# Optimization experiments

Hardware: AMD Instinct MI355X
Metric: run time of the kernel (lower is better)

## Reference

```python
import jax, jax.numpy as jnp
import numpy as np

B, N, K, H, G, C, P = 2, 8192, 16, 128, 256, 10, 8


def _w(key, fan_in, fan_out):
    return jax.random.normal(key, (fan_in, fan_out), jnp.float32) * (1.0 / np.sqrt(fan_in))


def setup_inputs() -> dict:
    key = jax.random.key(0)
    ks = jax.random.split(key, 24)
    inp = {
        "points": jax.random.normal(ks[0], (B, N, 3), jnp.float32),
        "normals": jax.random.normal(ks[1], (B, N, 3), jnp.float32),
        # point_encoder: Linear(6,H) -> ReLU -> Linear(H,H) -> ReLU
        "We1": _w(ks[2], 6, H), "be1": jnp.zeros((H,), jnp.float32),
        "We2": _w(ks[3], H, H), "be2": jnp.zeros((H,), jnp.float32),
        # local_mlp: Linear(2H,H) -> ReLU -> Linear(H,H) -> ReLU
        "Wl1": _w(ks[4], 2 * H, H), "bl1": jnp.zeros((H,), jnp.float32),
        "Wl2": _w(ks[5], H, H), "bl2": jnp.zeros((H,), jnp.float32),
        # context_proj: Linear(2H,G) -> ReLU
        "Wc": _w(ks[6], 2 * H, G), "bc": jnp.zeros((G,), jnp.float32),
        # classifier: Linear(2H+G,H) -> ReLU -> Linear(H,C)
        "Wk1": _w(ks[7], 2 * H + G, H), "bk1": jnp.zeros((H,), jnp.float32),
        "Wk2": _w(ks[8], H, C), "bk2": jnp.zeros((C,), jnp.float32),
        # param_head: Linear(2H+G,H) -> ReLU -> Linear(H,P)
        "Wp1": _w(ks[9], 2 * H + G, H), "bp1": jnp.zeros((H,), jnp.float32),
        "Wp2": _w(ks[10], H, P), "bp2": jnp.zeros((P,), jnp.float32),
        "k": K,
    }
    return inp


def _knn_indices(points, k):
    # squared pairwise distances (same ordering as torch.cdist); no grad needed
    pts = jax.lax.stop_gradient(points)
    sq = jnp.sum(pts * pts, axis=-1)                      # [B,N]
    d2 = sq[:, :, None] + sq[:, None, :] - 2.0 * jnp.einsum('bnc,bmc->bnm', pts, pts)
    _, idx = jax.lax.top_k(-d2, k + 1)                    # smallest k+1 distances
    return idx[:, :, 1:]                                  # drop self -> [B,N,k]


def _forward(points, normals, We1, be1, We2, be2, Wl1, bl1, Wl2, bl2,
             Wc, bc, Wk1, bk1, Wk2, bk2, Wp1, bp1, Wp2, bp2, k):
    x = jnp.concatenate([points, normals], axis=-1)       # [B,N,6]
    pf = jax.nn.relu(jax.nn.relu(x @ We1 + be1) @ We2 + be2)   # [B,N,H]

    idx = _knn_indices(points, k)                         # [B,N,k]
    nbr = jax.vmap(lambda f, i: f[i])(pf, idx)            # [B,N,k,H]
    ctr = pf[:, :, None, :]
    edge = jnp.concatenate([jnp.broadcast_to(ctr, nbr.shape), nbr - ctr], axis=-1)  # [B,N,k,2H]
    lf = jax.nn.relu(jax.nn.relu(edge @ Wl1 + bl1) @ Wl2 + bl2)
    lf = jnp.max(lf, axis=2)                              # [B,N,H]

    ctx = jax.nn.relu(jnp.concatenate([pf, lf], axis=-1) @ Wc + bc)  # [B,N,G]
    gf = jnp.max(ctx, axis=1, keepdims=True)              # [B,1,G]
    gf = jnp.broadcast_to(gf, (pf.shape[0], pf.shape[1], gf.shape[-1]))

    fused = jnp.concatenate([pf, lf, gf], axis=-1)        # [B,N,2H+G]
    logits = jax.nn.relu(fused @ Wk1 + bk1) @ Wk2 + bk2
    param_pred = jax.nn.relu(fused @ Wp1 + bp1) @ Wp2 + bp2
    return logits, param_pred


def reference(points, normals, We1, be1, We2, be2, Wl1, bl1, Wl2, bl2,
              Wc, bc, Wk1, bk1, Wk2, bk2, Wp1, bp1, Wp2, bp2, k):
    return _forward(points, normals, We1, be1, We2, be2, Wl1, bl1, Wl2, bl2,
                    Wc, bc, Wk1, bk1, Wk2, bk2, Wp1, bp1, Wp2, bp2, k)
```

## Files before the change

### kernel.cpp

```cpp
#include <hip/hip_runtime.h>

#define B_ 2
#define N_ 8192
#define NP 16384
#define K_ 16
#define H_ 128
#define KCAP 512

typedef short bf16x8 __attribute__((ext_vector_type(8)));
typedef float f32x4 __attribute__((ext_vector_type(4)));

__device__ inline unsigned short f2b(float f) {
    unsigned u = __builtin_bit_cast(unsigned, f);
    unsigned r = (u + 0x7fff + ((u >> 16) & 1)) >> 16;
    return (unsigned short)r;
}
__device__ inline bf16x8 ldb8(const unsigned short* p) {
    return *(const bf16x8*)p;
}
__device__ inline uint4 pack8(float4 a, float4 b) {
    uint4 pk;
    pk.x = (unsigned)f2b(a.x) | ((unsigned)f2b(a.y) << 16);
    pk.y = (unsigned)f2b(a.z) | ((unsigned)f2b(a.w) << 16);
    pk.z = (unsigned)f2b(b.x) | ((unsigned)f2b(b.y) << 16);
    pk.w = (unsigned)f2b(b.z) | ((unsigned)f2b(b.w) << 16);
    return pk;
}

__global__ __launch_bounds__(256) void k_h1(
    const float* __restrict__ pts, const float* __restrict__ nrm,
    const float* __restrict__ We1, const float* __restrict__ be1,
    unsigned short* __restrict__ h1, float* __restrict__ gf,
    float4* __restrict__ pts4) {
    int tid = blockIdx.x * 256 + threadIdx.x;
    if (blockIdx.x == 0) { gf[threadIdx.x] = 0.f; gf[256 + threadIdx.x] = 0.f; }
    if (tid < NP) {
        int p = tid;
        float x = pts[p * 3], y = pts[p * 3 + 1], z = pts[p * 3 + 2];
        float sq = __fadd_rn(__fadd_rn(__fmul_rn(x, x), __fmul_rn(y, y)), __fmul_rn(z, z));
        pts4[p] = make_float4(x, y, z, sq);
    }
    for (int o = tid; o < NP * 128; o += gridDim.x * 256) {
        int p = o >> 7, h = o & 127;
        float a = be1[h];
        a += pts[p * 3]     * We1[0 * 128 + h];
        a += pts[p * 3 + 1] * We1[1 * 128 + h];
        a += pts[p * 3 + 2] * We1[2 * 128 + h];
        a += nrm[p * 3]     * We1[3 * 128 + h];
        a += nrm[p * 3 + 1] * We1[4 * 128 + h];
        a += nrm[p * 3 + 2] * We1[5 * 128 + h];
        h1[o] = f2b(fmaxf(a, 0.f));
    }
}

__global__ __launch_bounds__(256) void k_prep(
    const float* __restrict__ Wl1, const float* __restrict__ bl1,
    const float* __restrict__ Wl2, const float* __restrict__ Wc,
    const float* __restrict__ Wk1, const float* __restrict__ Wp1,
    const float* __restrict__ We2,
    unsigned short* __restrict__ WuvT, float* __restrict__ bias_cat,
    unsigned short* __restrict__ Wl2T, unsigned short* __restrict__ WcT,
    unsigned short* __restrict__ Wk1T, unsigned short* __restrict__ Wp1T,
    unsigned short* __restrict__ We2T) {
    int tid = blockIdx.x * 256 + threadIdx.x;
    int stride = gridDim.x * 256;
    for (int i = tid; i < 256 * 128; i += stride) {
        int n = i >> 7, k = i & 127;
        float val = (n < 128) ? Wl1[k * 128 + n] - Wl1[(k + 128) * 128 + n]
                              : Wl1[(k + 128) * 128 + (n - 128)];
        WuvT[i] = f2b(val);
    }
    for (int i = tid; i < 256; i += stride) bias_cat[i] = (i < 128) ? bl1[i] : 0.f;
    for (int i = tid; i < 128 * 128; i += stride) {
        int n = i >> 7, k = i & 127;
        Wl2T[i] = f2b(Wl2[k * 128 + n]);
        We2T[i] = f2b(We2[k * 128 + n]);
    }
    for (int i = tid; i < 256 * 256; i += stride) {
        int n = i >> 8, k = i & 255;
        WcT[i] = f2b(Wc[k * 256 + n]);
    }
    for (int i = tid; i < 128 * 512; i += stride) {
        int n = i >> 9, k = i & 511;
        Wk1T[i] = f2b(Wk1[k * 128 + n]);
        Wp1T[i] = f2b(Wp1[k * 128 + n]);
    }
}

__global__ __launch_bounds__(256) void k_pf2(
    const unsigned short* __restrict__ h1, const unsigned short* __restrict__ We2T,
    const float* __restrict__ be2, float* __restrict__ pf) {
    int t = threadIdx.x, l = t & 63, w = t >> 6;
    int row0 = blockIdx.x * 64 + w * 16;
    f32x4 acc[8];
    #pragma unroll
    for (int nj = 0; nj < 8; ++nj) acc[nj] = (f32x4){0.f, 0.f, 0.f, 0.f};
    #pragma unroll
    for (int ks = 0; ks < 4; ++ks) {
        bf16x8 a = ldb8(&h1[(size_t)(row0 + (l & 15)) * 128 + ks * 32 + (l >> 4) * 8]);
        #pragma unroll
        for (int nj = 0; nj < 8; ++nj) {
            bf16x8 bfr = ldb8(&We2T[(size_t)(nj * 16 + (l & 15)) * 128 + ks * 32 + (l >> 4) * 8]);
            acc[nj] = __builtin_amdgcn_mfma_f32_16x16x32_bf16(a, bfr, acc[nj], 0, 0, 0);
        }
    }
    #pragma unroll
    for (int nj = 0; nj < 8; ++nj) {
        int col = nj * 16 + (l & 15);
        float bias = be2[col];
        #pragma unroll
        for (int rg = 0; rg < 4; ++rg) {
            int row = row0 + (l >> 4) * 4 + rg;
            pf[(size_t)row * 128 + col] = fmaxf(acc[nj][rg] + bias, 0.f);
        }
    }
}

__device__ inline float knn_thresh(const int* __restrict__ hh, int l) {
    int h0 = hh[4 * l], h1 = hh[4 * l + 1], h2 = hh[4 * l + 2], h3 = hh[4 * l + 3];
    int c0 = h0, c1 = c0 + h1, c2 = c1 + h2, c3 = c2 + h3;
    int tot = c3;
    int inc = tot;
    for (int off = 1; off < 64; off <<= 1) {
        int vv = __shfl_up(inc, off);
        if (l >= off) inc += vv;
    }
    int excl = inc - tot;
    int Bc = 255;
    if      (excl + c0 >= 16) Bc = 4 * l;
    else if (excl + c1 >= 16) Bc = 4 * l + 1;
    else if (excl + c2 >= 16) Bc = 4 * l + 2;
    else if (excl + c3 >= 16) Bc = 4 * l + 3;
    for (int m = 1; m < 64; m <<= 1) Bc = min(Bc, __shfl_xor(Bc, m));
    return __uint_as_float((unsigned)(Bc + 401) << 21);
}

__global__ __launch_bounds__(256) void k_knn(
    const float4* __restrict__ pts4, int* __restrict__ knn) {
    __shared__ int hist[4][2][260];
    __shared__ unsigned buf[4][2][KCAP];
    int t = threadIdx.x, w = t >> 6, l = t & 63;
    int b = blockIdx.x >> 10;
    int qbase = (blockIdx.x & 1023) * 8 + w * 2;
    const float4* pb = pts4 + b * N_;
    float4 qp0 = pb[qbase];
    float4 qp1 = pb[qbase + 1];
    for (int i = l; i < 520; i += 64) (&hist[w][0][0])[i] = 0;
    int cnt0 = 0, cnt1 = 0;

    float d2c0[16], d2c1[16];
    #pragma unroll
    for (int i = 0; i < 16; ++i) {
        int j = l + 64 * i;
        float4 c = pb[j];
        float dot0 = __fadd_rn(__fadd_rn(__fmul_rn(qp0.x, c.x), __fmul_rn(qp0.y, c.y)), __fmul_rn(qp0.z, c.z));
        float d20 = __fsub_rn(__fadd_rn(qp0.w, c.w), __fmul_rn(2.f, dot0));
        float dot1 = __fadd_rn(__fadd_rn(__fmul_rn(qp1.x, c.x), __fmul_rn(qp1.y, c.y)), __fmul_rn(qp1.z, c.z));
        float d21 = __fsub_rn(__fadd_rn(qp1.w, c.w), __fmul_rn(2.f, dot1));
        d2c0[i] = d20; d2c1[i] = d21;
        float hv0 = (j == qbase) ? 1e30f : d20;
        float hv1 = (j == qbase + 1) ? 1e30f : d21;
        unsigned u0 = __float_as_uint(hv0);
        int bk0 = (hv0 < 0.f) ? 0 : min(255, max(0, (int)(u0 >> 21) - 400));
        atomicAdd(&hist[w][0][bk0], 1);
        unsigned u1 = __float_as_uint(hv1);
        int bk1 = (hv1 < 0.f) ? 0 : min(255, max(0, (int)(u1 >> 21) - 400));
        atomicAdd(&hist[w][1][bk1], 1);
    }
    float Tf0 = knn_thresh(&hist[w][0][0], l);
    float Tf1 = knn_thresh(&hist[w][1][0], l);

    #pragma unroll
    for (int i = 0; i < 16; ++i) {
        int j = l + 64 * i;
        bool t0 = d2c0[i] < Tf0;
        unsigned long long m0 = __ballot(t0);
        if (t0) {
            int pos = cnt0 + __popcll(m0 & ((1ull << l) - 1ull));
            if (pos < KCAP) buf[w][0][pos] = (unsigned)j;
        }
        cnt0 += __popcll(m0);
        bool t1 = d2c1[i] < Tf1;
        unsigned long long m1 = __ballot(t1);
        if (t1) {
            int pos = cnt1 + __popcll(m1 & ((1ull << l) - 1ull));
            if (pos < KCAP) buf[w][1][pos] = (unsigned)j;
        }
        cnt1 += __popcll(m1);
    }

    #pragma unroll 2
    for (int i = 16; i < 128; ++i) {
        int j = l + 64 * i;
        float4 c = pb[j];
        float dot0 = __fadd_rn(__fadd_rn(__fmul_rn(qp0.x, c.x), __fmul_rn(qp0.y, c.y)), __fmul_rn(qp0.z, c.z));
        float d20 = __fsub_rn(__fadd_rn(qp0.w, c.w), __fmul_rn(2.f, dot0));
        float dot1 = __fadd_rn(__fadd_rn(__fmul_rn(qp1.x, c.x), __fmul_rn(qp1.y, c.y)), __fmul_rn(qp1.z, c.z));
        float d21 = __fsub_rn(__fadd_rn(qp1.w, c.w), __fmul_rn(2.f, dot1));
        bool t0 = d20 < Tf0;
        unsigned long long m0 = __ballot(t0);
        if (t0) {
            int pos = cnt0 + __popcll(m0 & ((1ull << l) - 1ull));
            if (pos < KCAP) buf[w][0][pos] = (unsigned)j;
        }
        cnt0 += __popcll(m0);
        bool t1 = d21 < Tf1;
        unsigned long long m1 = __ballot(t1);
        if (t1) {
            int pos = cnt1 + __popcll(m1 & ((1ull << l) - 1ull));
            if (pos < KCAP) buf[w][1][pos] = (unsigned)j;
        }
        cnt1 += __popcll(m1);
    }

    for (int qq = 0; qq < 2; ++qq) {
        int q = qbase + qq;
        float4 qp = qq ? qp1 : qp0;
        int m_ = min(qq ? cnt1 : cnt0, KCAP);
        unsigned long long key[8];
        #pragma unroll
        for (int r = 0; r < 8; ++r) {
            int e = l + 64 * r;
            if (e < m_) {
                int idx = (int)buf[w][qq][e];
                float4 c = pb[idx];
                float dot = __fadd_rn(__fadd_rn(__fmul_rn(qp.x, c.x), __fmul_rn(qp.y, c.y)), __fmul_rn(qp.z, c.z));
                float d2 = __fsub_rn(__fadd_rn(qp.w, c.w), __fmul_rn(2.f, dot));
                unsigned du = __float_as_uint(d2);
                unsigned mu = du ^ (unsigned)(((int)du >> 31) | 0x80000000);
                key[r] = ((unsigned long long)mu << 32) | (unsigned)idx;
            } else key[r] = ~0ull;
        }
        unsigned long long lmin = key[0];
        #pragma unroll
        for (int r = 1; r < 8; ++r) lmin = (key[r] < lmin) ? key[r] : lmin;
        int emitted = 0;
        for (int r17 = 0; r17 < 17 && emitted < 16; ++r17) {
            unsigned long long wv = lmin;
            for (int m = 1; m < 64; m <<= 1) {
                unsigned long long o = __shfl_xor(wv, m);
                wv = (o < wv) ? o : wv;
            }
            int idx = (int)(wv & 0xffffffffu);
            if (idx != q) {
                if (l == 0) knn[((size_t)b * N_ + q) * 16 + emitted] = b * N_ + idx;
                ++emitted;
            }
            if (lmin == wv) {
                #pragma unroll
                for (int r = 0; r < 8; ++r) if (key[r] == wv) key[r] = ~0ull;
                lmin = key[0];
                #pragma unroll
                for (int r = 1; r < 8; ++r) lmin = (key[r] < lmin) ? key[r] : lmin;
            }
        }
    }
}

__global__ __launch_bounds__(256) void k_uv(
    const float* __restrict__ pf, const unsigned short* __restrict__ WuvT,
    const float* __restrict__ bias_cat,
    float* __restrict__ u, float* __restrict__ v) {
    __shared__ __align__(16) unsigned short As[128 * 136];
    int t = threadIdx.x;
    int l = t & 63, w = t >> 6;
    int wr = w >> 1, wcn = w & 1;
    int rowbase = blockIdx.x * 128;
    int ncol0 = blockIdx.y * 128;

    #pragma unroll
    for (int i = 0; i < 8; ++i) {
        int ci = t + 256 * i;
        int r = ci >> 4, c8 = (ci & 15) * 8;
        const float4* sp = (const float4*)(pf + (size_t)(rowbase + r) * 128 + c8);
        *(uint4*)&As[r * 136 + c8] = pack8(sp[0], sp[1]);
    }
    __syncthreads();

    f32x4 acc[4][4];
    #pragma unroll
    for (int i = 0; i < 4; ++i)
        #pragma unroll
        for (int j = 0; j < 4; ++j) acc[i][j] = (f32x4){0.f, 0.f, 0.f, 0.f};

    #pragma unroll
    for (int ks = 0; ks < 4; ++ks) {
        bf16x8 bfr[4], afr[4];
        #pragma unroll
        for (int nj = 0; nj < 4; ++nj)
            bfr[nj] = ldb8(&WuvT[(size_t)(ncol0 + wcn * 64 + nj * 16 + (l & 15)) * 128 + ks * 32 + (l >> 4) * 8]);
        #pragma unroll
        for (int mi = 0; mi < 4; ++mi)
            afr[mi] = ldb8(&As[(wr * 64 + mi * 16 + (l & 15)) * 136 + ks * 32 + (l >> 4) * 8]);
        #pragma unroll
        for (int mi = 0; mi < 4; ++mi)
            #pragma unroll
            for (int nj = 0; nj < 4; ++nj)
                acc[mi][nj] = __builtin_amdgcn_mfma_f32_16x16x32_bf16(afr[mi], bfr[nj], acc[mi][nj], 0, 0, 0);
    }
    float* outp = (ncol0 == 0) ? u : v;
    #pragma unroll
    for (int mi = 0; mi < 4; ++mi)
        #pragma unroll
        for (int nj = 0; nj < 4; ++nj) {
            int col = wcn * 64 + nj * 16 + (l & 15);
            float bias = bias_cat[ncol0 + col];
            #pragma unroll
            for (int rg = 0; rg < 4; ++rg) {
                int row = wr * 64 + mi * 16 + (l >> 4) * 4 + rg;
                outp[(size_t)(rowbase + row) * 128 + col] = acc[mi][nj][rg] + bias;
            }
        }
}

__global__ __launch_bounds__(256) void k_edge(
    const float* __restrict__ u, const float* __restrict__ v,
    const int* __restrict__ knn, const unsigned short* __restrict__ Wl2T,
    const float* __restrict__ bl2, float* __restrict__ lf) {
    __shared__ __align__(16) unsigned short h1s[128 * 136];
    int t = threadIdx.x;
    int l = t & 63, w = t >> 6;
    int wr = w >> 1, wcn = w & 1;
    int rowbase = blockIdx.x * 128;
    int p0 = blockIdx.x * 8;

    #pragma unroll 2
    for (int i = 0; i < 8; ++i) {
        int ci = t + 256 * i;
        int r = ci >> 4, c8 = (ci & 15) * 8;
        int nb = knn[rowbase + r];
        int pt = p0 + (r >> 4);
        const float4* vp = (const float4*)(v + (size_t)nb * 128 + c8);
        const float4* up = (const float4*)(u + (size_t)pt * 128 + c8);
        float4 va = vp[0], vb = vp[1];
        float4 ua = up[0], ub = up[1];
        unsigned d0 = (unsigned)f2b(fmaxf(ua.x + va.x, 0.f)) | ((unsigned)f2b(fmaxf(ua.y + va.y, 0.f)) << 16);
        unsigned d1 = (unsigned)f2b(fmaxf(ua.z + va.z, 0.f)) | ((unsigned)f2b(fmaxf(ua.w + va.w, 0.f)) << 16);
        unsigned d2 = (unsigned)f2b(fmaxf(ub.x + vb.x, 0.f)) | ((unsigned)f2b(fmaxf(ub.y + vb.y, 0.f)) << 16);
        unsigned d3 = (unsigned)f2b(fmaxf(ub.z + vb.z, 0.f)) | ((unsigned)f2b(fmaxf(ub.w + vb.w, 0.f)) << 16);
        uint4 pk; pk.x = d0; pk.y = d1; pk.z = d2; pk.w = d3;
        *(uint4*)&h1s[r * 136 + c8] = pk;
    }
    __syncthreads();

    f32x4 acc[4][4];
    #pragma unroll
    for (int i = 0; i < 4; ++i)
        #pragma unroll
        for (int j = 0; j < 4; ++j) acc[i][j] = (f32x4){0.f, 0.f, 0.f, 0.f};

    #pragma unroll
    for (int ks = 0; ks < 4; ++ks) {
        bf16x8 bfr[4], afr[4];
        #pragma unroll
        for (int nj = 0; nj < 4; ++nj)
            bfr[nj] = ldb8(&Wl2T[(size_t)(wcn * 64 + nj * 16 + (l & 15)) * 128 + ks * 32 + (l >> 4) * 8]);
        #pragma unroll
        for (int mi = 0; mi < 4; ++mi)
            afr[mi] = ldb8(&h1s[(wr * 64 + mi * 16 + (l & 15)) * 136 + ks * 32 + (l >> 4) * 8]);
        #pragma unroll
        for (int mi = 0; mi < 4; ++mi)
            #pragma unroll
            for (int nj = 0; nj < 4; ++nj)
                acc[mi][nj] = __builtin_amdgcn_mfma_f32_16x16x32_bf16(afr[mi], bfr[nj], acc[mi][nj], 0, 0, 0);
    }

    #pragma unroll
    for (int mi = 0; mi < 4; ++mi)
        #pragma unroll
        for (int nj = 0; nj < 4; ++nj) {
            int col = wcn * 64 + nj * 16 + (l & 15);
            float bias = bl2[col];
            float m = fmaxf(acc[mi][nj][0] + bias, 0.f);
            m = fmaxf(m, fmaxf(acc[mi][nj][1] + bias, 0.f));
            m = fmaxf(m, fmaxf(acc[mi][nj][2] + bias, 0.f));
            m = fmaxf(m, fmaxf(acc[mi][nj][3] + bias, 0.f));
            m = fmaxf(m, __shfl_xor(m, 16));
            m = fmaxf(m, __shfl_xor(m, 32));
            if (l < 16) lf[(size_t)(p0 + wr * 4 + mi) * 128 + col] = m;
        }
}

__global__ __launch_bounds__(256) void k_ctx(
    const float* __restrict__ pf, const float* __restrict__ lf,
    const unsigned short* __restrict__ WcT, const float* __restrict__ bc,
    float* __restrict__ gf) {
    __shared__ __align__(16) unsigned short As[128 * 136];
    int t = threadIdx.x;
    int l = t & 63, w = t >> 6;
    int wr = w >> 1, wcn = w & 1;
    int rowbase = blockIdx.x * 128;
    int ncol0 = blockIdx.y * 128;
    int b = rowbase >> 13;

    f32x4 acc[4][4];
    #pragma unroll
    for (int i = 0; i < 4; ++i)
        #pragma unroll
        for (int j = 0; j < 4; ++j) acc[i][j] = (f32x4){0.f, 0.f, 0.f, 0.f};

    for (int kb = 0; kb < 2; ++kb) {
        const float* src = kb ? lf : pf;
        #pragma unroll
        for (int i = 0; i < 8; ++i) {
            int ci = t + 256 * i;
            int r = ci >> 4, c8 = (ci & 15) * 8;
            const float4* sp = (const float4*)(src + (size_t)(rowbase + r) * 128 + c8);
            *(uint4*)&As[r * 136 + c8] = pack8(sp[0], sp[1]);
        }
        __syncthreads();
        #pragma unroll
        for (int ks = 0; ks < 4; ++ks) {
            bf16x8 bfr[4], afr[4];
            #pragma unroll
            for (int nj = 0; nj < 4; ++nj)
                bfr[nj] = ldb8(&WcT[(size_t)(ncol0 + wcn * 64 + nj * 16 + (l & 15)) * 256 + kb * 128 + ks * 32 + (l >> 4) * 8]);
            #pragma unroll
            for (int mi = 0; mi < 4; ++mi)
                afr[mi] = ldb8(&As[(wr * 64 + mi * 16 + (l & 15)) * 136 + ks * 32 + (l >> 4) * 8]);
            #pragma unroll
            for (int mi = 0; mi < 4; ++mi)
                #pragma unroll
                for (int nj = 0; nj < 4; ++nj)
                    acc[mi][nj] = __builtin_amdgcn_mfma_f32_16x16x32_bf16(afr[mi], bfr[nj], acc[mi][nj], 0, 0, 0);
        }
        __syncthreads();
    }
    #pragma unroll
    for (int nj = 0; nj < 4; ++nj) {
        int col = ncol0 + wcn * 64 + nj * 16 + (l & 15);
        float m = acc[0][nj][0];
        #pragma unroll
        for (int mi = 0; mi < 4; ++mi)
            #pragma unroll
            for (int rg = 0; rg < 4; ++rg) m = fmaxf(m, acc[mi][nj][rg]);
        m = fmaxf(m + bc[col], 0.f);
        m = fmaxf(m, __shfl_xor(m, 16));
        m = fmaxf(m, __shfl_xor(m, 32));
        if (l < 16) atomicMax((unsigned int*)&gf[b * 256 + col], __float_as_uint(m));
    }
}

__global__ __launch_bounds__(256) void k_head(
    const float* __restrict__ pf, const float* __restrict__ lf, const float* __restrict__ gf,
    const unsigned short* __restrict__ Wk1T, const float* __restrict__ bk1,
    const float* __restrict__ Wk2, const float* __restrict__ bk2,
    const unsigned short* __restrict__ Wp1T, const float* __restrict__ bp1,
    const float* __restrict__ Wp2, const float* __restrict__ bp2,
    float* __restrict__ out) {
    __shared__ __align__(16) char smem[67584];
    unsigned short* As = (unsigned short*)smem;
    float* hs = (float*)smem;
    int t = threadIdx.x;
    int l = t & 63, w = t >> 6;
    int wr = w >> 1, wcn = w & 1;
    int rowbase = blockIdx.x * 128;
    int b = rowbase >> 13;
    int br = blockIdx.y;
    const unsigned short* W1T = br ? Wp1T : Wk1T;
    const float* b1 = br ? bp1 : bk1;
    const float* W2 = br ? Wp2 : Wk2;
    const float* b2p = br ? bp2 : bk2;
    int OC = br ? 8 : 10;
    float* obase = out + (br ? (size_t)NP * 10 : 0);

    f32x4 acc[4][4];
    #pragma unroll
    for (int i = 0; i < 4; ++i)
        #pragma unroll
        for (int j = 0; j < 4; ++j) acc[i][j] = (f32x4){0.f, 0.f, 0.f, 0.f};

    for (int kb = 0; kb < 4; ++kb) {
        #pragma unroll
        for (int i = 0; i < 8; ++i) {
            int ci = t + 256 * i;
            int r = ci >> 4, c8 = (ci & 15) * 8;
            const float4* sp;
            if (kb == 0)      sp = (const float4*)(pf + (size_t)(rowbase + r) * 128 + c8);
            else if (kb == 1) sp = (const float4*)(lf + (size_t)(rowbase + r) * 128 + c8);
            else              sp = (const float4*)(gf + b * 256 + (kb - 2) * 128 + c8);
            *(uint4*)&As[r * 136 + c8] = pack8(sp[0], sp[1]);
        }
        __syncthreads();
        #pragma unroll
        for (int ks = 0; ks < 4; ++ks) {
            bf16x8 bfr[4], afr[4];
            #pragma unroll
            for (int nj = 0; nj < 4; ++nj)
                bfr[nj] = ldb8(&W1T[(size_t)(wcn * 64 + nj * 16 + (l & 15)) * 512 + kb * 128 + ks * 32 + (l >> 4) * 8]);
            #pragma unroll
            for (int mi = 0; mi < 4; ++mi)
                afr[mi] = ldb8(&As[(wr * 64 + mi * 16 + (l & 15)) * 136 + ks * 32 + (l >> 4) * 8]);
            #pragma unroll
            for (int mi = 0; mi < 4; ++mi)
                #pragma unroll
                for (int nj = 0; nj < 4; ++nj)
                    acc[mi][nj] = __builtin_amdgcn_mfma_f32_16x16x32_bf16(afr[mi], bfr[nj], acc[mi][nj], 0, 0, 0);
        }
        __syncthreads();
    }
    #pragma unroll
    for (int mi = 0; mi < 4; ++mi)
        #pragma unroll
        for (int nj = 0; nj < 4; ++nj)
            #pragma unroll
            for (int rg = 0; rg < 4; ++rg) {
                int row = wr * 64 + mi * 16 + (l >> 4) * 4 + rg;
                int col = wcn * 64 + nj * 16 + (l & 15);
                hs[row * 132 + col] = fmaxf(acc[mi][nj][rg] + b1[col], 0.f);
            }
    __syncthreads();
    for (int o = t; o < 128 * OC; o += 256) {
        int r = o / OC, c = o % OC;
        float a = b2p[c];
        for (int k2 = 0; k2 < 128; ++k2) a += hs[r * 132 + k2] * W2[k2 * OC + c];
        obase[(size_t)(rowbase + r) * OC + c] = a;
    }
}

extern "C" void kernel_launch(void* const* d_in, const int* in_sizes, int n_in,
                              void* d_out, int out_size, void* d_ws, size_t ws_size,
                              hipStream_t stream) {
    const float* pts = (const float*)d_in[0];
    const float* nrm = (const float*)d_in[1];
    const float* We1 = (const float*)d_in[2];
    const float* be1 = (const float*)d_in[3];
    const float* We2 = (const float*)d_in[4];
    const float* be2 = (const float*)d_in[5];
    const float* Wl1 = (const float*)d_in[6];
    const float* bl1 = (const float*)d_in[7];
    const float* Wl2 = (const float*)d_in[8];
    const float* bl2 = (const float*)d_in[9];
    const float* Wc  = (const float*)d_in[10];
    const float* bc  = (const float*)d_in[11];
    const float* Wk1 = (const float*)d_in[12];
    const float* bk1 = (const float*)d_in[13];
    const float* Wk2 = (const float*)d_in[14];
    const float* bk2 = (const float*)d_in[15];
    const float* Wp1 = (const float*)d_in[16];
    const float* bp1 = (const float*)d_in[17];
    const float* Wp2 = (const float*)d_in[18];
    const float* bp2 = (const float*)d_in[19];
    float* out = (float*)d_out;

    char* ws = (char*)d_ws;
    size_t off = 0;
    float* pf = (float*)(ws + off);       off += (size_t)NP * 128 * 4;
    float* lf = (float*)(ws + off);       off += (size_t)NP * 128 * 4;
    float* u  = (float*)(ws + off);       off += (size_t)NP * 128 * 4;
    float* v  = (float*)(ws + off);       off += (size_t)NP * 128 * 4;
    int* knn  = (int*)(ws + off);         off += (size_t)NP * 16 * 4;
    float* gf = (float*)(ws + off);       off += 2048;
    float4* pts4 = (float4*)(ws + off);   off += (size_t)NP * 16;
    float* bias_cat = (float*)(ws + off); off += 1024;
    unsigned short* WuvT = (unsigned short*)(ws + off); off += 256 * 128 * 2;
    unsigned short* Wl2T = (unsigned short*)(ws + off); off += 128 * 128 * 2;
    unsigned short* WcT  = (unsigned short*)(ws + off); off += 256 * 256 * 2;
    unsigned short* Wk1T = (unsigned short*)(ws + off); off += 128 * 512 * 2;
    unsigned short* Wp1T = (unsigned short*)(ws + off); off += 128 * 512 * 2;
    unsigned short* We2T = (unsigned short*)(ws + off); off += 128 * 128 * 2;
    unsigned short* h1   = (unsigned short*)(ws + off); off += (size_t)NP * 128 * 2;

    hipLaunchKernelGGL(k_h1, dim3(2048), dim3(256), 0, stream,
                       pts, nrm, We1, be1, h1, gf, pts4);
    hipLaunchKernelGGL(k_prep, dim3(64), dim3(256), 0, stream,
                       Wl1, bl1, Wl2, Wc, Wk1, Wp1, We2,
                       WuvT, bias_cat, Wl2T, WcT, Wk1T, Wp1T, We2T);
    hipLaunchKernelGGL(k_knn, dim3(2048), dim3(256), 0, stream, pts4, knn);
    hipLaunchKernelGGL(k_pf2, dim3(256), dim3(256), 0, stream,
                       h1, We2T, be2, pf);
    hipLaunchKernelGGL(k_uv, dim3(128, 2), dim3(256), 0, stream,
                       pf, WuvT, bias_cat, u, v);
    hipLaunchKernelGGL(k_edge, dim3(2048), dim3(256), 0, stream,
                       u, v, knn, Wl2T, bl2, lf);
    hipLaunchKernelGGL(k_ctx, dim3(128, 2), dim3(256), 0, stream,
                       pf, lf, WcT, bc, gf);
    hipLaunchKernelGGL(k_head, dim3(128, 2), dim3(256), 0, stream,
                       pf, lf, gf, Wk1T, bk1, Wk2, bk2, Wp1T, bp1, Wp2, bp2, out);
}
```

Measured before the change: 358.0 us.

## Process one kNN query per wave and store distance keys in candidate buffer

The kNN kernel now gives each wavefront one query point instead of two, and the grid doubles to 4096 blocks. Candidates passing the histogram threshold are stored as packed 64-bit (distance, index) keys, so the final selection no longer reloads points or recomputes distances. The histogram pass no longer keeps per-lane distances in registers, which lowers register pressure. The trade-off is that every candidate point load is now shared by only one query instead of two, doubling point reads and distance work per query.

```diff
diff --git a/kernel.cpp b/kernel.cpp
--- a/kernel.cpp
+++ b/kernel.cpp
@@ -137,122 +137,74 @@
 
 __global__ __launch_bounds__(256) void k_knn(
     const float4* __restrict__ pts4, int* __restrict__ knn) {
-    __shared__ int hist[4][2][260];
-    __shared__ unsigned buf[4][2][KCAP];
+    __shared__ int hist[4][260];
+    __shared__ unsigned long long buf[4][KCAP];
     int t = threadIdx.x, w = t >> 6, l = t & 63;
-    int b = blockIdx.x >> 10;
-    int qbase = (blockIdx.x & 1023) * 8 + w * 2;
+    int b = blockIdx.x >> 11;
+    int q = (blockIdx.x & 2047) * 4 + w;
     const float4* pb = pts4 + b * N_;
-    float4 qp0 = pb[qbase];
-    float4 qp1 = pb[qbase + 1];
-    for (int i = l; i < 520; i += 64) (&hist[w][0][0])[i] = 0;
-    int cnt0 = 0, cnt1 = 0;
-
-    float d2c0[16], d2c1[16];
-    #pragma unroll
+    float4 qp = pb[q];
+    for (int i = l; i < 256; i += 64) hist[w][i] = 0;
+    int cntw = 0;
+
+    #pragma unroll 2
     for (int i = 0; i < 16; ++i) {
         int j = l + 64 * i;
         float4 c = pb[j];
-        float dot0 = __fadd_rn(__fadd_rn(__fmul_rn(qp0.x, c.x), __fmul_rn(qp0.y, c.y)), __fmul_rn(qp0.z, c.z));
-        float d20 = __fsub_rn(__fadd_rn(qp0.w, c.w), __fmul_rn(2.f, dot0));
-        float dot1 = __fadd_rn(__fadd_rn(__fmul_rn(qp1.x, c.x), __fmul_rn(qp1.y, c.y)), __fmul_rn(qp1.z, c.z));
-        float d21 = __fsub_rn(__fadd_rn(qp1.w, c.w), __fmul_rn(2.f, dot1));
-        d2c0[i] = d20; d2c1[i] = d21;
-        float hv0 = (j == qbase) ? 1e30f : d20;
-        float hv1 = (j == qbase + 1) ? 1e30f : d21;
-        unsigned u0 = __float_as_uint(hv0);
-        int bk0 = (hv0 < 0.f) ? 0 : min(255, max(0, (int)(u0 >> 21) - 400));
-        atomicAdd(&hist[w][0][bk0], 1);
-        unsigned u1 = __float_as_uint(hv1);
-        int bk1 = (hv1 < 0.f) ? 0 : min(255, max(0, (int)(u1 >> 21) - 400));
-        atomicAdd(&hist[w][1][bk1], 1);
-    }
-    float Tf0 = knn_thresh(&hist[w][0][0], l);
-    float Tf1 = knn_thresh(&hist[w][1][0], l);
-
-    #pragma unroll
-    for (int i = 0; i < 16; ++i) {
-        int j = l + 64 * i;
-        bool t0 = d2c0[i] < Tf0;
-        unsigned long long m0 = __ballot(t0);
-        if (t0) {
-            int pos = cnt0 + __popcll(m0 & ((1ull << l) - 1ull));
-            if (pos < KCAP) buf[w][0][pos] = (unsigned)j;
-        }
-        cnt0 += __popcll(m0);
-        bool t1 = d2c1[i] < Tf1;
-        unsigned long long m1 = __ballot(t1);
-        if (t1) {
-            int pos = cnt1 + __popcll(m1 & ((1ull << l) - 1ull));
-            if (pos < KCAP) buf[w][1][pos] = (unsigned)j;
-        }
-        cnt1 += __popcll(m1);
-    }
-
-    #pragma unroll 2
-    for (int i = 16; i < 128; ++i) {
+        float dot = __fadd_rn(__fadd_rn(__fmul_rn(qp.x, c.x), __fmul_rn(qp.y, c.y)), __fmul_rn(qp.z, c.z));
+        float d2 = __fsub_rn(__fadd_rn(qp.w, c.w), __fmul_rn(2.f, dot));
+        d2 = (j == q) ? 1e30f : d2;
+        unsigned uu = __float_as_uint(d2);
+        int bk = (d2 < 0.f) ? 0 : min(255, max(0, (int)(uu >> 21) - 400));
+        atomicAdd(&hist[w][bk], 1);
+    }
+    float Tf = knn_thresh(&hist[w][0], l);
+
+    #pragma unroll 4
+    for (int i = 0; i < 128; ++i) {
         int j = l + 64 * i;
         float4 c = pb[j];
-        float dot0 = __fadd_rn(__fadd_rn(__fmul_rn(qp0.x, c.x), __fmul_rn(qp0.y, c.y)), __fmul_rn(qp0.z, c.z));
-        float d20 = __fsub_rn(__fadd_rn(qp0.w, c.w), __fmul_rn(2.f, dot0));
-        float dot1 = __fadd_rn(__fadd_rn(__fmul_rn(qp1.x, c.x), __fmul_rn(qp1.y, c.y)), __fmul_rn(qp1.z, c.z));
-        float d21 = __fsub_rn(__fadd_rn(qp1.w, c.w), __fmul_rn(2.f, dot1));
-        bool t0 = d20 < Tf0;
-        unsigned long long m0 = __ballot(t0);
-        if (t0) {
-            int pos = cnt0 + __popcll(m0 & ((1ull << l) - 1ull));
-            if (pos < KCAP) buf[w][0][pos] = (unsigned)j;
-        }
-        cnt0 += __popcll(m0);
-        bool t1 = d21 < Tf1;
-        unsigned long long m1 = __ballot(t1);
-        if (t1) {
-            int pos = cnt1 + __popcll(m1 & ((1ull << l) - 1ull));
-            if (pos < KCAP) buf[w][1][pos] = (unsigned)j;
-        }
-        cnt1 += __popcll(m1);
-    }
-
-    for (int qq = 0; qq < 2; ++qq) {
-        int q = qbase + qq;
-        float4 qp = qq ? qp1 : qp0;
-        int m_ = min(qq ? cnt1 : cnt0, KCAP);
-        unsigned long long key[8];
-        #pragma unroll
-        for (int r = 0; r < 8; ++r) {
-            int e = l + 64 * r;
-            if (e < m_) {
-                int idx = (int)buf[w][qq][e];
-                float4 c = pb[idx];
-                float dot = __fadd_rn(__fadd_rn(__fmul_rn(qp.x, c.x), __fmul_rn(qp.y, c.y)), __fmul_rn(qp.z, c.z));
-                float d2 = __fsub_rn(__fadd_rn(qp.w, c.w), __fmul_rn(2.f, dot));
-                unsigned du = __float_as_uint(d2);
-                unsigned mu = du ^ (unsigned)(((int)du >> 31) | 0x80000000);
-                key[r] = ((unsigned long long)mu << 32) | (unsigned)idx;
-            } else key[r] = ~0ull;
-        }
-        unsigned long long lmin = key[0];
-        #pragma unroll
-        for (int r = 1; r < 8; ++r) lmin = (key[r] < lmin) ? key[r] : lmin;
-        int emitted = 0;
-        for (int r17 = 0; r17 < 17 && emitted < 16; ++r17) {
-            unsigned long long wv = lmin;
-            for (int m = 1; m < 64; m <<= 1) {
-                unsigned long long o = __shfl_xor(wv, m);
-                wv = (o < wv) ? o : wv;
-            }
-            int idx = (int)(wv & 0xffffffffu);
-            if (idx != q) {
-                if (l == 0) knn[((size_t)b * N_ + q) * 16 + emitted] = b * N_ + idx;
-                ++emitted;
-            }
-            if (lmin == wv) {
-                #pragma unroll
-                for (int r = 0; r < 8; ++r) if (key[r] == wv) key[r] = ~0ull;
-                lmin = key[0];
-                #pragma unroll
-                for (int r = 1; r < 8; ++r) lmin = (key[r] < lmin) ? key[r] : lmin;
-            }
+        float dot = __fadd_rn(__fadd_rn(__fmul_rn(qp.x, c.x), __fmul_rn(qp.y, c.y)), __fmul_rn(qp.z, c.z));
+        float d2 = __fsub_rn(__fadd_rn(qp.w, c.w), __fmul_rn(2.f, dot));
+        bool take = (d2 < Tf);
+        unsigned long long mask = __ballot(take);
+        if (take) {
+            unsigned du = __float_as_uint(d2);
+            unsigned mu = du ^ (unsigned)(((int)du >> 31) | 0x80000000);
+            int pos = cntw + __popcll(mask & ((1ull << l) - 1ull));
+            if (pos < KCAP) buf[w][pos] = ((unsigned long long)mu << 32) | (unsigned)j;
+        }
+        cntw += __popcll(mask);
+    }
+    int m_ = min(cntw, KCAP);
+
+    unsigned long long key[8];
+    #pragma unroll
+    for (int r = 0; r < 8; ++r) {
+        int e = l + 64 * r;
+        key[r] = (e < m_) ? buf[w][e] : ~0ull;
+    }
+    unsigned long long lmin = key[0];
+    #pragma unroll
+    for (int r = 1; r < 8; ++r) lmin = (key[r] < lmin) ? key[r] : lmin;
+    int emitted = 0;
+    for (int r17 = 0; r17 < 17 && emitted < 16; ++r17) {
+        unsigned long long wv = lmin;
+        for (int m = 1; m < 64; m <<= 1) {
+            unsigned long long o = __shfl_xor(wv, m);
+            wv = (o < wv) ? o : wv;
+        }
+        int idx = (int)(wv & 0xffffffffu);
+        if (idx != q) {
+            if (l == 0) knn[((size_t)b * N_ + q) * 16 + emitted] = b * N_ + idx;
+            ++emitted;
+        }
+        if (lmin == wv) {
+            #pragma unroll
+            for (int r = 0; r < 8; ++r) if (key[r] == wv) key[r] = ~0ull;
+            lmin = key[0];
+            #pragma unroll
+            for (int r = 1; r < 8; ++r) lmin = (key[r] < lmin) ? key[r] : lmin;
         }
     }
 }
@@ -566,7 +518,7 @@
     hipLaunchKernelGGL(k_prep, dim3(64), dim3(256), 0, stream,
                        Wl1, bl1, Wl2, Wc, Wk1, Wp1, We2,
                        WuvT, bias_cat, Wl2T, WcT, Wk1T, Wp1T, We2T);
-    hipLaunchKernelGGL(k_knn, dim3(2048), dim3(256), 0, stream, pts4, knn);
+    hipLaunchKernelGGL(k_knn, dim3(4096), dim3(256), 0, stream, pts4, knn);
     hipLaunchKernelGGL(k_pf2, dim3(256), dim3(256), 0, stream,
                        h1, We2T, be2, pf);
     hipLaunchKernelGGL(k_uv, dim3(128, 2), dim3(256), 0, stream,
```

After: 349.1 us. 1.03x faster.
